# Kernel optimization log

Hardware: AMD Instinct MI355X
Metric: run time of the kernel (lower is better)

## Reference

```python
import jax, jax.numpy as jnp
import numpy as np

N_NODES = 100352
NUM_GRAPHS = 512
NODES_PER_GRAPH = 196  # N_NODES / NUM_GRAPHS, equal-size graphs
N_EDGES = 1605632
IN_C, HID_C, OUT_C, K = 128, 64, 32, 30


def setup_inputs() -> dict:
    key = jax.random.key(0)
    ks = jax.random.split(key, 4)
    x = jax.random.normal(ks[0], (N_NODES, IN_C), dtype=jnp.float32)
    edge_index = jax.random.randint(ks[1], (2, N_EDGES), 0, N_NODES, dtype=jnp.int32)
    batch = jnp.repeat(jnp.arange(NUM_GRAPHS, dtype=jnp.int32), NODES_PER_GRAPH)
    W1 = jax.random.normal(ks[2], (IN_C, HID_C), jnp.float32) * (1.0 / np.sqrt(IN_C))
    b1 = jnp.zeros((HID_C,), jnp.float32)
    W2 = jax.random.normal(ks[3], (HID_C, OUT_C), jnp.float32) * (1.0 / np.sqrt(HID_C))
    b2 = jnp.zeros((OUT_C,), jnp.float32)
    return dict(x=x, edge_index=edge_index, batch=batch, W1=W1, b1=b1, W2=W2, b2=b2)


def gcn_conv(x, src, dst, W, b, num_nodes):
    # PyG GCNConv: xW, add self-loops, symmetric normalization, scatter-add to dst.
    xw = x @ W  # [N, D_out]
    deg = jax.ops.segment_sum(jnp.ones_like(dst, dtype=xw.dtype), dst,
                              num_segments=num_nodes) + 1.0  # +1 for self-loop
    dis = jax.lax.rsqrt(deg)  # deg^{-1/2}
    msg = (dis[src] * dis[dst])[:, None] * xw[src]  # [E, D_out]
    out = jax.ops.segment_sum(msg, dst, num_segments=num_nodes)
    out = out + (dis * dis)[:, None] * xw  # self-loop term deg^{-1} * xw
    return out + b


def sort_pool(x, batch, num_graphs, max_nodes, k):
    # PyG SortAggregation: dense per-graph batch, sort nodes desc by last channel, top-k, zero padding.
    N, D = x.shape
    fill = x.min() - 1.0
    counts = jax.ops.segment_sum(jnp.ones((N,), jnp.int32), batch, num_segments=num_graphs)
    starts = jnp.cumsum(counts) - counts  # exclusive prefix sum
    pos = jnp.arange(N, dtype=jnp.int32) - starts[batch]
    dense = jnp.full((num_graphs, max_nodes, D), fill, x.dtype).at[batch, pos].set(x)
    order = jnp.argsort(-dense[:, :, -1], axis=1)[:, :k]  # [B, k] top-k by last channel
    topk = jnp.take_along_axis(dense, order[:, :, None], axis=1)  # [B, k, D]
    topk = jnp.where(topk == fill, jnp.zeros((), x.dtype), topk)
    return topk.reshape(num_graphs, k * D)


def reference(x, edge_index, batch, W1, b1, W2, b2):
    src, dst = edge_index[0], edge_index[1]
    n = x.shape[0]
    h = jax.nn.relu(gcn_conv(x, src, dst, W1, b1, n))
    h = gcn_conv(h, src, dst, W2, b2, n)
    return sort_pool(h, batch, NUM_GRAPHS, NODES_PER_GRAPH, K)
```

## Files before the change

### kernel.cpp

```cpp
#include <hip/hip_runtime.h>

#define N_NODES   100352
#define N_EDGES   1605632
#define IN_C      128
#define HID_C     64
#define OUT_C     32
#define NUM_GRAPHS 512
#define NPG       196
#define TOPK      30

#define NB        196
#define BCAP      10240
#define LCAP      10240

typedef float v16f __attribute__((ext_vector_type(16)));

#define OFF_DEG     0u
#define OFF_ROWPTR  401408u
#define OFF_DIS     802816u
#define OFF_BCNT    1204224u
#define OFF_ARENA   1206272u
#define OFF_CSR     17262592u
#define OFF_XW1     23685120u
#define OFF_H       49375232u
#define OFF_XW2     75065344u

__global__ __launch_bounds__(256) void k_bucket(const int* __restrict__ src, const int* __restrict__ dst,
                                                int* __restrict__ bucket_cnt, int* __restrict__ arena) {
    __shared__ int hist[NB];
    __shared__ int cur[NB];
    int tid = threadIdx.x;
    for (int i = tid; i < NB; i += 256) hist[i] = 0;
    __syncthreads();
    int base4 = blockIdx.x * 2048 + tid;
#pragma unroll
    for (int r = 0; r < 8; ++r) {
        int4 d = ((const int4*)dst)[base4 + r * 256];
        atomicAdd(&hist[d.x >> 9], 1);
        atomicAdd(&hist[d.y >> 9], 1);
        atomicAdd(&hist[d.z >> 9], 1);
        atomicAdd(&hist[d.w >> 9], 1);
    }
    __syncthreads();
    for (int i = tid; i < NB; i += 256) {
        int c = hist[i];
        cur[i] = (c > 0) ? atomicAdd(&bucket_cnt[i], c) : 0;
    }
    __syncthreads();
#pragma unroll
    for (int r = 0; r < 8; ++r) {
        int4 s = ((const int4*)src)[base4 + r * 256];
        int4 d = ((const int4*)dst)[base4 + r * 256];
        int p0 = atomicAdd(&cur[d.x >> 9], 1);
        int p1 = atomicAdd(&cur[d.y >> 9], 1);
        int p2 = atomicAdd(&cur[d.z >> 9], 1);
        int p3 = atomicAdd(&cur[d.w >> 9], 1);
        if (p0 < BCAP) arena[(size_t)(d.x >> 9) * BCAP + p0] = (s.x << 9) | (d.x & 511);
        if (p1 < BCAP) arena[(size_t)(d.y >> 9) * BCAP + p1] = (s.y << 9) | (d.y & 511);
        if (p2 < BCAP) arena[(size_t)(d.z >> 9) * BCAP + p2] = (s.z << 9) | (d.z & 511);
        if (p3 < BCAP) arena[(size_t)(d.w >> 9) * BCAP + p3] = (s.w << 9) | (d.w & 511);
    }
}

__global__ __launch_bounds__(256) void k_build(const int* __restrict__ arena, const int* __restrict__ bucket_cnt,
                                               int* __restrict__ row_ptr,
                                               int* __restrict__ deg, float* __restrict__ dis,
                                               int* __restrict__ csr_src) {
    __shared__ int bsc[256];
    __shared__ int dloc[512];
    __shared__ int sc[512];
    __shared__ int cur[512];
    __shared__ int stage[LCAP];
    int b = blockIdx.x;
    int tid = threadIdx.x;
    int bv = (tid < NB) ? bucket_cnt[tid] : 0;
    bsc[tid] = bv;
    __syncthreads();
    for (int o = 1; o < 256; o <<= 1) {
        int a = (tid >= o) ? bsc[tid - o] : 0;
        __syncthreads();
        bsc[tid] += a;
        __syncthreads();
    }
    int nb = min(bucket_cnt[b], BCAP);
    int gbase = bsc[b] - bucket_cnt[b];
    const int* ap = arena + (size_t)b * BCAP;
    for (int i = tid; i < 512; i += 256) dloc[i] = 0;
    __syncthreads();
    for (int i = tid; i < nb; i += 256) {
        int e = ap[i];
        atomicAdd(&dloc[e & 511], 1);
    }
    __syncthreads();
    for (int i = tid; i < 512; i += 256) sc[i] = dloc[i];
    __syncthreads();
    for (int o = 1; o < 512; o <<= 1) {
        int i0 = tid, i1 = tid + 256;
        int v0 = (i0 >= o) ? sc[i0 - o] : 0;
        int v1 = (i1 >= o) ? sc[i1 - o] : 0;
        __syncthreads();
        sc[i0] += v0;
        sc[i1] += v1;
        __syncthreads();
    }
    for (int i = tid; i < 512; i += 256) {
        int d = dloc[i];
        int off = sc[i] - d;
        int node = b * 512 + i;
        row_ptr[node] = gbase + off;
        deg[node] = d;
        dis[node] = (float)(1.0 / sqrt((double)(d + 1)));
        cur[i] = off;
    }
    __syncthreads();
    bool inlds = (nb <= LCAP);
    for (int i = tid; i < nb; i += 256) {
        int e = ap[i];
        int p = atomicAdd(&cur[e & 511], 1);
        int sv = ((unsigned)e) >> 9;
        if (inlds) stage[p] = sv;
        else       csr_src[gbase + p] = sv;
    }
    __syncthreads();
    if (inlds)
        for (int i = tid; i < nb; i += 256) csr_src[gbase + i] = stage[i];
}

__global__ __launch_bounds__(256) void k_mm1(const float* __restrict__ x, const float* __restrict__ W1,
                                             const float* __restrict__ dis, float* __restrict__ xw1s) {
    int tid = threadIdx.x;
    int n = blockIdx.x * 64 + (tid & 63);
    int ch = __builtin_amdgcn_readfirstlane((tid >> 6) * 16);
    const float4* xrow = (const float4*)(x + (size_t)n * IN_C);
    float acc[16];
#pragma unroll
    for (int c = 0; c < 16; ++c) acc[c] = 0.f;
    float4 xq = xrow[0];
#pragma unroll 1
    for (int q = 0; q < IN_C / 4; ++q) {
        float4 xn = xrow[(q + 1) & (IN_C / 4 - 1)];
        const float* wp = W1 + q * 4 * HID_C + ch;
        v16f w0, w1, w2, w3;
        asm volatile("s_load_dwordx16 %0, %1, 0x0"   : "=s"(w0) : "s"(wp));
        asm volatile("s_load_dwordx16 %0, %1, 0x100" : "=s"(w1) : "s"(wp));
        asm volatile("s_load_dwordx16 %0, %1, 0x200" : "=s"(w2) : "s"(wp));
        asm volatile("s_load_dwordx16 %0, %1, 0x300" : "=s"(w3) : "s"(wp));
        asm volatile("s_waitcnt lgkmcnt(0)" : "+s"(w0), "+s"(w1), "+s"(w2), "+s"(w3));
#pragma unroll
        for (int c = 0; c < 16; ++c) {
            acc[c] = fmaf(xq.x, w0[c], acc[c]);
            acc[c] = fmaf(xq.y, w1[c], acc[c]);
            acc[c] = fmaf(xq.z, w2[c], acc[c]);
            acc[c] = fmaf(xq.w, w3[c], acc[c]);
        }
        xq = xn;
    }
    float dv = dis[n];
    float4* orow = (float4*)(xw1s + (size_t)n * HID_C + ch);
#pragma unroll
    for (int c4 = 0; c4 < 4; ++c4) {
        float4 o;
        o.x = acc[4 * c4 + 0] * dv;
        o.y = acc[4 * c4 + 1] * dv;
        o.z = acc[4 * c4 + 2] * dv;
        o.w = acc[4 * c4 + 3] * dv;
        orow[c4] = o;
    }
}

__global__ __launch_bounds__(256) void k_agg1(const float* __restrict__ xw1s, const int* __restrict__ csr_src,
                                              const int* __restrict__ row_ptr, const int* __restrict__ deg,
                                              const float* __restrict__ dis, const float* __restrict__ b1,
                                              float* __restrict__ h) {
    int lane = threadIdx.x & 63;
    int v = blockIdx.x * 4 + (threadIdx.x >> 6);
    int start = row_ptr[v];
    int cnt = deg[v];
    float acc0 = xw1s[(size_t)v * HID_C + lane];
    float acc1 = 0.f, acc2 = 0.f, acc3 = 0.f;
    for (int base = 0; base < cnt; base += 64) {
        int mcnt = min(64, cnt - base);
        int sj = 0;
        if (lane < mcnt) sj = csr_src[start + base + lane];
        int j = 0;
        for (; j + 8 <= mcnt; j += 8) {
            int s0 = __shfl(sj, j + 0), s1 = __shfl(sj, j + 1);
            int s2 = __shfl(sj, j + 2), s3 = __shfl(sj, j + 3);
            int s4 = __shfl(sj, j + 4), s5 = __shfl(sj, j + 5);
            int s6 = __shfl(sj, j + 6), s7 = __shfl(sj, j + 7);
            float v0 = xw1s[(size_t)s0 * HID_C + lane];
            float v1 = xw1s[(size_t)s1 * HID_C + lane];
            float v2 = xw1s[(size_t)s2 * HID_C + lane];
            float v3 = xw1s[(size_t)s3 * HID_C + lane];
            float v4 = xw1s[(size_t)s4 * HID_C + lane];
            float v5 = xw1s[(size_t)s5 * HID_C + lane];
            float v6 = xw1s[(size_t)s6 * HID_C + lane];
            float v7 = xw1s[(size_t)s7 * HID_C + lane];
            acc0 += v0 + v4;
            acc1 += v1 + v5;
            acc2 += v2 + v6;
            acc3 += v3 + v7;
        }
        for (; j < mcnt; ++j) {
            int s = __shfl(sj, j);
            acc0 += xw1s[(size_t)s * HID_C + lane];
        }
    }
    float o = fmaf(dis[v], (acc0 + acc1) + (acc2 + acc3), b1[lane]);
    h[(size_t)v * HID_C + lane] = fmaxf(o, 0.f);
}

__global__ __launch_bounds__(256) void k_mm2(const float* __restrict__ h, const float* __restrict__ W2,
                                             const float* __restrict__ dis, float* __restrict__ xw2s) {
    int tid = threadIdx.x;
    int n = blockIdx.x * 128 + (tid & 127);
    int ch = __builtin_amdgcn_readfirstlane((tid >> 7) * 16);
    const float4* hrow = (const float4*)(h + (size_t)n * HID_C);
    float acc[16];
#pragma unroll
    for (int c = 0; c < 16; ++c) acc[c] = 0.f;
    float4 xq = hrow[0];
#pragma unroll 1
    for (int q = 0; q < HID_C / 4; ++q) {
        float4 xn = hrow[(q + 1) & (HID_C / 4 - 1)];
        const float* wp = W2 + q * 4 * OUT_C + ch;
        v16f w0, w1, w2, w3;
        asm volatile("s_load_dwordx16 %0, %1, 0x0"   : "=s"(w0) : "s"(wp));
        asm volatile("s_load_dwordx16 %0, %1, 0x80"  : "=s"(w1) : "s"(wp));
        asm volatile("s_load_dwordx16 %0, %1, 0x100" : "=s"(w2) : "s"(wp));
        asm volatile("s_load_dwordx16 %0, %1, 0x180" : "=s"(w3) : "s"(wp));
        asm volatile("s_waitcnt lgkmcnt(0)" : "+s"(w0), "+s"(w1), "+s"(w2), "+s"(w3));
#pragma unroll
        for (int c = 0; c < 16; ++c) {
            acc[c] = fmaf(xq.x, w0[c], acc[c]);
            acc[c] = fmaf(xq.y, w1[c], acc[c]);
            acc[c] = fmaf(xq.z, w2[c], acc[c]);
            acc[c] = fmaf(xq.w, w3[c], acc[c]);
        }
        xq = xn;
    }
    float dv = dis[n];
    float4* orow = (float4*)(xw2s + (size_t)n * OUT_C + ch);
#pragma unroll
    for (int c4 = 0; c4 < 4; ++c4) {
        float4 o;
        o.x = acc[4 * c4 + 0] * dv;
        o.y = acc[4 * c4 + 1] * dv;
        o.z = acc[4 * c4 + 2] * dv;
        o.w = acc[4 * c4 + 3] * dv;
        orow[c4] = o;
    }
}

__global__ __launch_bounds__(512) void k_agg2sort(const float* __restrict__ xw2s, const int* __restrict__ csr_src,
                                                  const int* __restrict__ row_ptr, const int* __restrict__ deg,
                                                  const float* __restrict__ dis, const float* __restrict__ b2,
                                                  float* __restrict__ out) {
    __shared__ float o2[NPG][OUT_C];
    __shared__ float keys[NPG];
    __shared__ int order[TOPK];
    int g = blockIdx.x;
    int tid = threadIdx.x;
    int lane = tid & 31;
    int grp = tid >> 5;
    for (int i = grp; i < NPG; i += 16) {
        int v = g * NPG + i;
        int start = row_ptr[v];
        int cnt = deg[v];
        float acc0 = xw2s[(size_t)v * OUT_C + lane];
        float acc1 = 0.f, acc2 = 0.f, acc3 = 0.f;
        for (int base = 0; base < cnt; base += 32) {
            int mcnt = min(32, cnt - base);
            int sj = 0;
            if (lane < mcnt) sj = csr_src[start + base + lane];
            int j = 0;
            for (; j + 8 <= mcnt; j += 8) {
                int s0 = __shfl(sj, j + 0, 32), s1 = __shfl(sj, j + 1, 32);
                int s2 = __shfl(sj, j + 2, 32), s3 = __shfl(sj, j + 3, 32);
                int s4 = __shfl(sj, j + 4, 32), s5 = __shfl(sj, j + 5, 32);
                int s6 = __shfl(sj, j + 6, 32), s7 = __shfl(sj, j + 7, 32);
                float v0 = xw2s[(size_t)s0 * OUT_C + lane];
                float v1 = xw2s[(size_t)s1 * OUT_C + lane];
                float v2 = xw2s[(size_t)s2 * OUT_C + lane];
                float v3 = xw2s[(size_t)s3 * OUT_C + lane];
                float v4 = xw2s[(size_t)s4 * OUT_C + lane];
                float v5 = xw2s[(size_t)s5 * OUT_C + lane];
                float v6 = xw2s[(size_t)s6 * OUT_C + lane];
                float v7 = xw2s[(size_t)s7 * OUT_C + lane];
                acc0 += v0 + v4;
                acc1 += v1 + v5;
                acc2 += v2 + v6;
                acc3 += v3 + v7;
            }
            for (; j < mcnt; ++j) {
                int s = __shfl(sj, j, 32);
                acc0 += xw2s[(size_t)s * OUT_C + lane];
            }
        }
        float val = fmaf(dis[v], (acc0 + acc1) + (acc2 + acc3), b2[lane]);
        o2[i][lane] = val;
        if (lane == OUT_C - 1) keys[i] = val;
    }
    __syncthreads();
    for (int i = tid; i < NPG; i += 512) {
        float my = keys[i];
        int r = 0;
        for (int j = 0; j < NPG; ++j) {
            float kj = keys[j];
            r += (kj > my) || (kj == my && j < i);
        }
        if (r < TOPK) order[r] = i;
    }
    __syncthreads();
    for (int idx = tid; idx < TOPK * OUT_C; idx += 512) {
        int r = idx >> 5;
        int c = idx & 31;
        out[g * (TOPK * OUT_C) + idx] = o2[order[r]][c];
    }
}

extern "C" void kernel_launch(void* const* d_in, const int* in_sizes, int n_in,
                              void* d_out, int out_size, void* d_ws, size_t ws_size,
                              hipStream_t stream) {
    const float* x  = (const float*)d_in[0];
    const int*   ei = (const int*)d_in[1];
    const int*   srcp = ei;
    const int*   dstp = ei + N_EDGES;
    const float* W1 = (const float*)d_in[3];
    const float* b1 = (const float*)d_in[4];
    const float* W2 = (const float*)d_in[5];
    const float* b2 = (const float*)d_in[6];
    float* out = (float*)d_out;

    char* w = (char*)d_ws;
    int*    deg      = (int*)(w + OFF_DEG);
    int*    row_ptr  = (int*)(w + OFF_ROWPTR);
    float*  dis      = (float*)(w + OFF_DIS);
    int*    bcnt     = (int*)(w + OFF_BCNT);
    int*    arena    = (int*)(w + OFF_ARENA);
    int*    csr_src  = (int*)(w + OFF_CSR);
    float*  xw1s     = (float*)(w + OFF_XW1);
    float*  h        = (float*)(w + OFF_H);
    float*  xw2s     = (float*)(w + OFF_XW2);

    hipMemsetAsync(bcnt, 0, NB * sizeof(int), stream);
    k_bucket<<<N_EDGES / (256 * 32), 256, 0, stream>>>(srcp, dstp, bcnt, arena);
    k_build <<<NB, 256, 0, stream>>>(arena, bcnt, row_ptr, deg, dis, csr_src);
    k_mm1   <<<N_NODES / 64, 256, 0, stream>>>(x, W1, dis, xw1s);
    k_agg1  <<<N_NODES / 4, 256, 0, stream>>>(xw1s, csr_src, row_ptr, deg, dis, b1, h);
    k_mm2   <<<N_NODES / 128, 256, 0, stream>>>(h, W2, dis, xw2s);
    k_agg2sort<<<NUM_GRAPHS, 512, 0, stream>>>(xw2s, csr_src, row_ptr, deg, dis, b2, out);
}
```

Measured before the change: 224.8 us.

## Store layer-1 features in channel-group-major layout and regroup aggregation per 8-channel slice

The layer-1 projection and hidden activations are now stored as eight channel-group planes of 8 floats per node, and the first aggregation kernel assigns each block to one plane. Each wavefront handles 8 edges at a time with 8 lanes per edge, so each gathered row is a 32-byte slice and a plane is small enough to stay cache-resident. The aim is to improve cache locality of the random neighbour gathers. The bucketing kernel also reads 8 contiguous edges per thread with src and dst loaded once and uses 4x more blocks. The trade-offs are more passes over the CSR indices (once per group), a cross-lane reduction per node, and strided reads in mm2.

```diff
diff --git a/kernel.cpp b/kernel.cpp
--- a/kernel.cpp
+++ b/kernel.cpp
@@ -32,15 +32,14 @@
     int tid = threadIdx.x;
     for (int i = tid; i < NB; i += 256) hist[i] = 0;
     __syncthreads();
-    int base4 = blockIdx.x * 2048 + tid;
-#pragma unroll
-    for (int r = 0; r < 8; ++r) {
-        int4 d = ((const int4*)dst)[base4 + r * 256];
-        atomicAdd(&hist[d.x >> 9], 1);
-        atomicAdd(&hist[d.y >> 9], 1);
-        atomicAdd(&hist[d.z >> 9], 1);
-        atomicAdd(&hist[d.w >> 9], 1);
-    }
+    int e0 = (blockIdx.x * 256 + tid) * 8;
+    int4 sa = ((const int4*)src)[e0 / 4], sb = ((const int4*)src)[e0 / 4 + 1];
+    int4 da = ((const int4*)dst)[e0 / 4], db = ((const int4*)dst)[e0 / 4 + 1];
+    int es[8] = {sa.x, sa.y, sa.z, sa.w, sb.x, sb.y, sb.z, sb.w};
+    int ed[8] = {da.x, da.y, da.z, da.w, db.x, db.y, db.z, db.w};
+    int eb[8];
+#pragma unroll
+    for (int j = 0; j < 8; ++j) { eb[j] = ed[j] >> 9; atomicAdd(&hist[eb[j]], 1); }
     __syncthreads();
     for (int i = tid; i < NB; i += 256) {
         int c = hist[i];
@@ -48,17 +47,9 @@
     }
     __syncthreads();
 #pragma unroll
-    for (int r = 0; r < 8; ++r) {
-        int4 s = ((const int4*)src)[base4 + r * 256];
-        int4 d = ((const int4*)dst)[base4 + r * 256];
-        int p0 = atomicAdd(&cur[d.x >> 9], 1);
-        int p1 = atomicAdd(&cur[d.y >> 9], 1);
-        int p2 = atomicAdd(&cur[d.z >> 9], 1);
-        int p3 = atomicAdd(&cur[d.w >> 9], 1);
-        if (p0 < BCAP) arena[(size_t)(d.x >> 9) * BCAP + p0] = (s.x << 9) | (d.x & 511);
-        if (p1 < BCAP) arena[(size_t)(d.y >> 9) * BCAP + p1] = (s.y << 9) | (d.y & 511);
-        if (p2 < BCAP) arena[(size_t)(d.z >> 9) * BCAP + p2] = (s.z << 9) | (d.z & 511);
-        if (p3 < BCAP) arena[(size_t)(d.w >> 9) * BCAP + p3] = (s.w << 9) | (d.w & 511);
+    for (int j = 0; j < 8; ++j) {
+        int p = atomicAdd(&cur[eb[j]], 1);
+        if (p < BCAP) arena[(size_t)eb[j] * BCAP + p] = (es[j] << 9) | (ed[j] & 511);
     }
 }
 
@@ -127,7 +118,7 @@
 }
 
 __global__ __launch_bounds__(256) void k_mm1(const float* __restrict__ x, const float* __restrict__ W1,
-                                             const float* __restrict__ dis, float* __restrict__ xw1s) {
+                                             const float* __restrict__ dis, float* __restrict__ xw1cs) {
     int tid = threadIdx.x;
     int n = blockIdx.x * 64 + (tid & 63);
     int ch = __builtin_amdgcn_readfirstlane((tid >> 6) * 16);
@@ -156,73 +147,70 @@
         xq = xn;
     }
     float dv = dis[n];
-    float4* orow = (float4*)(xw1s + (size_t)n * HID_C + ch);
-#pragma unroll
-    for (int c4 = 0; c4 < 4; ++c4) {
-        float4 o;
-        o.x = acc[4 * c4 + 0] * dv;
-        o.y = acc[4 * c4 + 1] * dv;
-        o.z = acc[4 * c4 + 2] * dv;
-        o.w = acc[4 * c4 + 3] * dv;
-        orow[c4] = o;
-    }
-}
-
-__global__ __launch_bounds__(256) void k_agg1(const float* __restrict__ xw1s, const int* __restrict__ csr_src,
+    int g0 = ch >> 3;
+    float4* o0 = (float4*)(xw1cs + ((size_t)g0 * N_NODES + n) * 8);
+    float4* o1 = (float4*)(xw1cs + ((size_t)(g0 + 1) * N_NODES + n) * 8);
+    o0[0] = make_float4(acc[0] * dv, acc[1] * dv, acc[2] * dv, acc[3] * dv);
+    o0[1] = make_float4(acc[4] * dv, acc[5] * dv, acc[6] * dv, acc[7] * dv);
+    o1[0] = make_float4(acc[8] * dv, acc[9] * dv, acc[10] * dv, acc[11] * dv);
+    o1[1] = make_float4(acc[12] * dv, acc[13] * dv, acc[14] * dv, acc[15] * dv);
+}
+
+__global__ __launch_bounds__(256) void k_agg1(const float* __restrict__ xw1cs, const int* __restrict__ csr_src,
                                               const int* __restrict__ row_ptr, const int* __restrict__ deg,
                                               const float* __restrict__ dis, const float* __restrict__ b1,
-                                              float* __restrict__ h) {
-    int lane = threadIdx.x & 63;
-    int v = blockIdx.x * 4 + (threadIdx.x >> 6);
-    int start = row_ptr[v];
-    int cnt = deg[v];
-    float acc0 = xw1s[(size_t)v * HID_C + lane];
-    float acc1 = 0.f, acc2 = 0.f, acc3 = 0.f;
-    for (int base = 0; base < cnt; base += 64) {
-        int mcnt = min(64, cnt - base);
-        int sj = 0;
-        if (lane < mcnt) sj = csr_src[start + base + lane];
-        int j = 0;
-        for (; j + 8 <= mcnt; j += 8) {
-            int s0 = __shfl(sj, j + 0), s1 = __shfl(sj, j + 1);
-            int s2 = __shfl(sj, j + 2), s3 = __shfl(sj, j + 3);
-            int s4 = __shfl(sj, j + 4), s5 = __shfl(sj, j + 5);
-            int s6 = __shfl(sj, j + 6), s7 = __shfl(sj, j + 7);
-            float v0 = xw1s[(size_t)s0 * HID_C + lane];
-            float v1 = xw1s[(size_t)s1 * HID_C + lane];
-            float v2 = xw1s[(size_t)s2 * HID_C + lane];
-            float v3 = xw1s[(size_t)s3 * HID_C + lane];
-            float v4 = xw1s[(size_t)s4 * HID_C + lane];
-            float v5 = xw1s[(size_t)s5 * HID_C + lane];
-            float v6 = xw1s[(size_t)s6 * HID_C + lane];
-            float v7 = xw1s[(size_t)s7 * HID_C + lane];
-            acc0 += v0 + v4;
-            acc1 += v1 + v5;
-            acc2 += v2 + v6;
-            acc3 += v3 + v7;
-        }
-        for (; j < mcnt; ++j) {
-            int s = __shfl(sj, j);
-            acc0 += xw1s[(size_t)s * HID_C + lane];
-        }
-    }
-    float o = fmaf(dis[v], (acc0 + acc1) + (acc2 + acc3), b1[lane]);
-    h[(size_t)v * HID_C + lane] = fmaxf(o, 0.f);
-}
-
-__global__ __launch_bounds__(256) void k_mm2(const float* __restrict__ h, const float* __restrict__ W2,
+                                              float* __restrict__ hcs) {
+    int tid = threadIdx.x;
+    int g = blockIdx.x & 7;
+    int nb = blockIdx.x >> 3;
+    int lane = tid & 63;
+    int esub = lane >> 3;
+    int c = lane & 7;
+    const float* xg = xw1cs + (size_t)g * N_NODES * 8;
+    float* hg = hcs + (size_t)g * N_NODES * 8;
+    float bv = b1[g * 8 + c];
+    int v0 = nb * 64 + (tid >> 6) * 16;
+#pragma unroll 1
+    for (int i = 0; i < 16; ++i) {
+        int v = v0 + i;
+        int start = row_ptr[v];
+        int cnt = deg[v];
+        float acc0 = (esub == 0) ? xg[(size_t)v * 8 + c] : 0.f;
+        float acc1 = 0.f;
+        int base = 0;
+        for (; base + 16 <= cnt; base += 16) {
+            int e = start + base + esub;
+            int s0 = csr_src[e];
+            int s1 = csr_src[e + 8];
+            acc0 += xg[(size_t)s0 * 8 + c];
+            acc1 += xg[(size_t)s1 * 8 + c];
+        }
+        for (; base < cnt; base += 8) {
+            int idx = base + esub;
+            if (idx < cnt) acc0 += xg[(size_t)csr_src[start + idx] * 8 + c];
+        }
+        float acc = acc0 + acc1;
+        acc += __shfl_xor(acc, 8);
+        acc += __shfl_xor(acc, 16);
+        acc += __shfl_xor(acc, 32);
+        float o = fmaf(dis[v], acc, bv);
+        if (lane < 8) hg[(size_t)v * 8 + c] = fmaxf(o, 0.f);
+    }
+}
+
+__global__ __launch_bounds__(256) void k_mm2(const float* __restrict__ hcs, const float* __restrict__ W2,
                                              const float* __restrict__ dis, float* __restrict__ xw2s) {
     int tid = threadIdx.x;
     int n = blockIdx.x * 128 + (tid & 127);
     int ch = __builtin_amdgcn_readfirstlane((tid >> 7) * 16);
-    const float4* hrow = (const float4*)(h + (size_t)n * HID_C);
+    float4 xq = *(const float4*)(hcs + (size_t)n * 8);
     float acc[16];
 #pragma unroll
     for (int c = 0; c < 16; ++c) acc[c] = 0.f;
-    float4 xq = hrow[0];
 #pragma unroll 1
     for (int q = 0; q < HID_C / 4; ++q) {
-        float4 xn = hrow[(q + 1) & (HID_C / 4 - 1)];
+        int qn = (q + 1) & (HID_C / 4 - 1);
+        float4 xn = *(const float4*)(hcs + ((size_t)(qn >> 1) * N_NODES + n) * 8 + (qn & 1) * 4);
         const float* wp = W2 + q * 4 * OUT_C + ch;
         v16f w0, w1, w2, w3;
         asm volatile("s_load_dwordx16 %0, %1, 0x0"   : "=s"(w0) : "s"(wp));
@@ -339,15 +327,15 @@
     int*    bcnt     = (int*)(w + OFF_BCNT);
     int*    arena    = (int*)(w + OFF_ARENA);
     int*    csr_src  = (int*)(w + OFF_CSR);
-    float*  xw1s     = (float*)(w + OFF_XW1);
-    float*  h        = (float*)(w + OFF_H);
+    float*  xw1cs    = (float*)(w + OFF_XW1);
+    float*  hcs      = (float*)(w + OFF_H);
     float*  xw2s     = (float*)(w + OFF_XW2);
 
     hipMemsetAsync(bcnt, 0, NB * sizeof(int), stream);
-    k_bucket<<<N_EDGES / (256 * 32), 256, 0, stream>>>(srcp, dstp, bcnt, arena);
+    k_bucket<<<N_EDGES / (256 * 8), 256, 0, stream>>>(srcp, dstp, bcnt, arena);
     k_build <<<NB, 256, 0, stream>>>(arena, bcnt, row_ptr, deg, dis, csr_src);
-    k_mm1   <<<N_NODES / 64, 256, 0, stream>>>(x, W1, dis, xw1s);
-    k_agg1  <<<N_NODES / 4, 256, 0, stream>>>(xw1s, csr_src, row_ptr, deg, dis, b1, h);
-    k_mm2   <<<N_NODES / 128, 256, 0, stream>>>(h, W2, dis, xw2s);
+    k_mm1   <<<N_NODES / 64, 256, 0, stream>>>(x, W1, dis, xw1cs);
+    k_agg1  <<<8 * (N_NODES / 64), 256, 0, stream>>>(xw1cs, csr_src, row_ptr, deg, dis, b1, hcs);
+    k_mm2   <<<N_NODES / 128, 256, 0, stream>>>(hcs, W2, dis, xw2s);
     k_agg2sort<<<NUM_GRAPHS, 512, 0, stream>>>(xw2s, csr_src, row_ptr, deg, dis, b2, out);
 }
```

Measured after the change: 357.9 us. +59.2%, slower.

## Merge edge bucketing and first matmul into one launch, scale separately

Applied to the files above, without the earlier changes.

Edge bucketing and the x@W1 matmul now run in one launch, using disjoint block ranges, so the two independent stages can overlap on the GPU. Because the matmul no longer waits for degrees, the deg^-1/2 scaling moves into a new elementwise k_scale kernel that runs after k_build. Bucketing blocks now handle 8 edges per thread across 784 blocks instead of 32 edges per thread. The cost is an extra read and write pass over the 25MB xw1 buffer plus one more kernel launch.

```diff
diff --git a/kernel.cpp b/kernel.cpp
--- a/kernel.cpp
+++ b/kernel.cpp
@@ -12,6 +12,7 @@
 #define NB        196
 #define BCAP      10240
 #define LCAP      10240
+#define NBUCKET_BLOCKS 784
 
 typedef float v16f __attribute__((ext_vector_type(16)));
 
@@ -25,40 +26,73 @@
 #define OFF_H       49375232u
 #define OFF_XW2     75065344u
 
-__global__ __launch_bounds__(256) void k_bucket(const int* __restrict__ src, const int* __restrict__ dst,
-                                                int* __restrict__ bucket_cnt, int* __restrict__ arena) {
-    __shared__ int hist[NB];
-    __shared__ int cur[NB];
+__global__ __launch_bounds__(256) void k_phase1(const int* __restrict__ src, const int* __restrict__ dst,
+                                                int* __restrict__ bucket_cnt, int* __restrict__ arena,
+                                                const float* __restrict__ x, const float* __restrict__ W1,
+                                                float* __restrict__ xw1) {
     int tid = threadIdx.x;
-    for (int i = tid; i < NB; i += 256) hist[i] = 0;
-    __syncthreads();
-    int base4 = blockIdx.x * 2048 + tid;
-#pragma unroll
-    for (int r = 0; r < 8; ++r) {
-        int4 d = ((const int4*)dst)[base4 + r * 256];
-        atomicAdd(&hist[d.x >> 9], 1);
-        atomicAdd(&hist[d.y >> 9], 1);
-        atomicAdd(&hist[d.z >> 9], 1);
-        atomicAdd(&hist[d.w >> 9], 1);
-    }
-    __syncthreads();
-    for (int i = tid; i < NB; i += 256) {
-        int c = hist[i];
-        cur[i] = (c > 0) ? atomicAdd(&bucket_cnt[i], c) : 0;
-    }
-    __syncthreads();
-#pragma unroll
-    for (int r = 0; r < 8; ++r) {
-        int4 s = ((const int4*)src)[base4 + r * 256];
-        int4 d = ((const int4*)dst)[base4 + r * 256];
-        int p0 = atomicAdd(&cur[d.x >> 9], 1);
-        int p1 = atomicAdd(&cur[d.y >> 9], 1);
-        int p2 = atomicAdd(&cur[d.z >> 9], 1);
-        int p3 = atomicAdd(&cur[d.w >> 9], 1);
-        if (p0 < BCAP) arena[(size_t)(d.x >> 9) * BCAP + p0] = (s.x << 9) | (d.x & 511);
-        if (p1 < BCAP) arena[(size_t)(d.y >> 9) * BCAP + p1] = (s.y << 9) | (d.y & 511);
-        if (p2 < BCAP) arena[(size_t)(d.z >> 9) * BCAP + p2] = (s.z << 9) | (d.z & 511);
-        if (p3 < BCAP) arena[(size_t)(d.w >> 9) * BCAP + p3] = (s.w << 9) | (d.w & 511);
+    if (blockIdx.x < NBUCKET_BLOCKS) {
+        __shared__ int hist[NB];
+        __shared__ int cur[NB];
+        for (int i = tid; i < NB; i += 256) hist[i] = 0;
+        __syncthreads();
+        int e0 = (blockIdx.x * 256 + tid) * 8;
+        int4 sa = ((const int4*)src)[e0 / 4], sb = ((const int4*)src)[e0 / 4 + 1];
+        int4 da = ((const int4*)dst)[e0 / 4], db = ((const int4*)dst)[e0 / 4 + 1];
+        int es[8] = {sa.x, sa.y, sa.z, sa.w, sb.x, sb.y, sb.z, sb.w};
+        int ed[8] = {da.x, da.y, da.z, da.w, db.x, db.y, db.z, db.w};
+        int eb[8];
+#pragma unroll
+        for (int j = 0; j < 8; ++j) { eb[j] = ed[j] >> 9; atomicAdd(&hist[eb[j]], 1); }
+        __syncthreads();
+        for (int i = tid; i < NB; i += 256) {
+            int c = hist[i];
+            cur[i] = (c > 0) ? atomicAdd(&bucket_cnt[i], c) : 0;
+        }
+        __syncthreads();
+#pragma unroll
+        for (int j = 0; j < 8; ++j) {
+            int p = atomicAdd(&cur[eb[j]], 1);
+            if (p < BCAP) arena[(size_t)eb[j] * BCAP + p] = (es[j] << 9) | (ed[j] & 511);
+        }
+    } else {
+        int bid = blockIdx.x - NBUCKET_BLOCKS;
+        int n = bid * 64 + (tid & 63);
+        int ch = __builtin_amdgcn_readfirstlane((tid >> 6) * 16);
+        const float4* xrow = (const float4*)(x + (size_t)n * IN_C);
+        float acc[16];
+#pragma unroll
+        for (int c = 0; c < 16; ++c) acc[c] = 0.f;
+        float4 xq = xrow[0];
+#pragma unroll 1
+        for (int q = 0; q < IN_C / 4; ++q) {
+            float4 xn = xrow[(q + 1) & (IN_C / 4 - 1)];
+            const float* wp = W1 + q * 4 * HID_C + ch;
+            v16f w0, w1, w2, w3;
+            asm volatile("s_load_dwordx16 %0, %1, 0x0"   : "=s"(w0) : "s"(wp));
+            asm volatile("s_load_dwordx16 %0, %1, 0x100" : "=s"(w1) : "s"(wp));
+            asm volatile("s_load_dwordx16 %0, %1, 0x200" : "=s"(w2) : "s"(wp));
+            asm volatile("s_load_dwordx16 %0, %1, 0x300" : "=s"(w3) : "s"(wp));
+            asm volatile("s_waitcnt lgkmcnt(0)" : "+s"(w0), "+s"(w1), "+s"(w2), "+s"(w3));
+#pragma unroll
+            for (int c = 0; c < 16; ++c) {
+                acc[c] = fmaf(xq.x, w0[c], acc[c]);
+                acc[c] = fmaf(xq.y, w1[c], acc[c]);
+                acc[c] = fmaf(xq.z, w2[c], acc[c]);
+                acc[c] = fmaf(xq.w, w3[c], acc[c]);
+            }
+            xq = xn;
+        }
+        float4* orow = (float4*)(xw1 + (size_t)n * HID_C + ch);
+#pragma unroll
+        for (int c4 = 0; c4 < 4; ++c4) {
+            float4 o;
+            o.x = acc[4 * c4 + 0];
+            o.y = acc[4 * c4 + 1];
+            o.z = acc[4 * c4 + 2];
+            o.w = acc[4 * c4 + 3];
+            orow[c4] = o;
+        }
     }
 }
 
@@ -126,45 +160,14 @@
         for (int i = tid; i < nb; i += 256) csr_src[gbase + i] = stage[i];
 }
 
-__global__ __launch_bounds__(256) void k_mm1(const float* __restrict__ x, const float* __restrict__ W1,
-                                             const float* __restrict__ dis, float* __restrict__ xw1s) {
-    int tid = threadIdx.x;
-    int n = blockIdx.x * 64 + (tid & 63);
-    int ch = __builtin_amdgcn_readfirstlane((tid >> 6) * 16);
-    const float4* xrow = (const float4*)(x + (size_t)n * IN_C);
-    float acc[16];
-#pragma unroll
-    for (int c = 0; c < 16; ++c) acc[c] = 0.f;
-    float4 xq = xrow[0];
-#pragma unroll 1
-    for (int q = 0; q < IN_C / 4; ++q) {
-        float4 xn = xrow[(q + 1) & (IN_C / 4 - 1)];
-        const float* wp = W1 + q * 4 * HID_C + ch;
-        v16f w0, w1, w2, w3;
-        asm volatile("s_load_dwordx16 %0, %1, 0x0"   : "=s"(w0) : "s"(wp));
-        asm volatile("s_load_dwordx16 %0, %1, 0x100" : "=s"(w1) : "s"(wp));
-        asm volatile("s_load_dwordx16 %0, %1, 0x200" : "=s"(w2) : "s"(wp));
-        asm volatile("s_load_dwordx16 %0, %1, 0x300" : "=s"(w3) : "s"(wp));
-        asm volatile("s_waitcnt lgkmcnt(0)" : "+s"(w0), "+s"(w1), "+s"(w2), "+s"(w3));
-#pragma unroll
-        for (int c = 0; c < 16; ++c) {
-            acc[c] = fmaf(xq.x, w0[c], acc[c]);
-            acc[c] = fmaf(xq.y, w1[c], acc[c]);
-            acc[c] = fmaf(xq.z, w2[c], acc[c]);
-            acc[c] = fmaf(xq.w, w3[c], acc[c]);
-        }
-        xq = xn;
-    }
-    float dv = dis[n];
-    float4* orow = (float4*)(xw1s + (size_t)n * HID_C + ch);
-#pragma unroll
-    for (int c4 = 0; c4 < 4; ++c4) {
-        float4 o;
-        o.x = acc[4 * c4 + 0] * dv;
-        o.y = acc[4 * c4 + 1] * dv;
-        o.z = acc[4 * c4 + 2] * dv;
-        o.w = acc[4 * c4 + 3] * dv;
-        orow[c4] = o;
+__global__ __launch_bounds__(256) void k_scale(float* __restrict__ xw1, const float* __restrict__ dis) {
+    int idx = blockIdx.x * 256 + threadIdx.x;
+    float4* p = (float4*)xw1;
+    for (int i = idx; i < N_NODES * (HID_C / 4); i += gridDim.x * 256) {
+        float d = dis[i >> 4];
+        float4 v = p[i];
+        v.x *= d; v.y *= d; v.z *= d; v.w *= d;
+        p[i] = v;
     }
 }
 
@@ -339,15 +342,15 @@
     int*    bcnt     = (int*)(w + OFF_BCNT);
     int*    arena    = (int*)(w + OFF_ARENA);
     int*    csr_src  = (int*)(w + OFF_CSR);
-    float*  xw1s     = (float*)(w + OFF_XW1);
+    float*  xw1      = (float*)(w + OFF_XW1);
     float*  h        = (float*)(w + OFF_H);
     float*  xw2s     = (float*)(w + OFF_XW2);
 
     hipMemsetAsync(bcnt, 0, NB * sizeof(int), stream);
-    k_bucket<<<N_EDGES / (256 * 32), 256, 0, stream>>>(srcp, dstp, bcnt, arena);
+    k_phase1<<<NBUCKET_BLOCKS + N_NODES / 64, 256, 0, stream>>>(srcp, dstp, bcnt, arena, x, W1, xw1);
     k_build <<<NB, 256, 0, stream>>>(arena, bcnt, row_ptr, deg, dis, csr_src);
-    k_mm1   <<<N_NODES / 64, 256, 0, stream>>>(x, W1, dis, xw1s);
-    k_agg1  <<<N_NODES / 4, 256, 0, stream>>>(xw1s, csr_src, row_ptr, deg, dis, b1, h);
+    k_scale <<<2048, 256, 0, stream>>>(xw1, dis);
+    k_agg1  <<<N_NODES / 4, 256, 0, stream>>>(xw1, csr_src, row_ptr, deg, dis, b1, h);
     k_mm2   <<<N_NODES / 128, 256, 0, stream>>>(h, W2, dis, xw2s);
     k_agg2sort<<<NUM_GRAPHS, 512, 0, stream>>>(xw2s, csr_src, row_ptr, deg, dis, b2, out);
 }
```

Measured after the change: 236.5 us. 5.2% more time.
